# Optimization experiments

Hardware: AMD Instinct MI355X
Metric: run time of the kernel (lower is better)

Reference implementation:

```python
import jax, jax.numpy as jnp
import numpy as np

EMBED_DIM = 1024
NUM_HEADS = 16
HEAD_DIM = EMBED_DIM // NUM_HEADS


def setup_inputs() -> dict:
    key = jax.random.key(0)
    ks = jax.random.split(key, 9)
    B, S, D = 2, 2048, EMBED_DIM
    scale = 1.0 / np.sqrt(D)
    x = jax.random.normal(ks[0], (B, S, D), dtype=jnp.float32)
    # nn.Linear weights are [out, in]; store as [in, out] for x @ W
    Wq = jax.random.uniform(ks[1], (D, D), jnp.float32, -scale, scale)
    bq = jax.random.uniform(ks[2], (D,), jnp.float32, -scale, scale)
    Wk = jax.random.uniform(ks[3], (D, D), jnp.float32, -scale, scale)
    bk = jax.random.uniform(ks[4], (D,), jnp.float32, -scale, scale)
    Wv = jax.random.uniform(ks[5], (D, D), jnp.float32, -scale, scale)
    bv = jax.random.uniform(ks[6], (D,), jnp.float32, -scale, scale)
    Wo = jax.random.uniform(ks[7], (D, D), jnp.float32, -scale, scale)
    bo = jax.random.uniform(ks[8], (D,), jnp.float32, -scale, scale)
    return {"x": x, "Wq": Wq, "bq": bq, "Wk": Wk, "bk": bk,
            "Wv": Wv, "bv": bv, "Wo": Wo, "bo": bo}


def reference(x, Wq, bq, Wk, bk, Wv, bv, Wo, bo):
    B, S, D = x.shape
    H, Dh = NUM_HEADS, HEAD_DIM
    q = (x @ Wq + bq).reshape(B, S, H, Dh).transpose(0, 2, 1, 3)  # [B,H,S,Dh]
    k = (x @ Wk + bk).reshape(B, S, H, Dh).transpose(0, 2, 1, 3)
    v = (x @ Wv + bv).reshape(B, S, H, Dh).transpose(0, 2, 1, 3)
    scores = jnp.einsum('bhqd,bhkd->bhqk', q, k) / jnp.sqrt(jnp.float32(Dh))
    attn = jax.nn.softmax(scores, axis=-1)
    out = jnp.einsum('bhqk,bhkd->bhqd', attn, v)  # [B,H,S,Dh]
    out = out.transpose(0, 2, 1, 3).reshape(B, S, D)
    return out @ Wo + bo
```

## Files before the change

kernel.cpp:

```cpp
#include <hip/hip_runtime.h>
#include <hip/hip_bf16.h>
#include <stdint.h>

using f32x4 = __attribute__((ext_vector_type(4))) float;
using s16x8 = __attribute__((ext_vector_type(8))) short;
using s16x4 = __attribute__((ext_vector_type(4))) short;

__device__ __forceinline__ unsigned short f2bf(float f) {
  union { float f; unsigned int u; } v; v.f = f;
  return (unsigned short)((v.u + 0x7FFFu + ((v.u >> 16) & 1u)) >> 16);
}

__device__ __forceinline__ float exp2_(float x) {
  float r;
  asm("v_exp_f32 %0, %1" : "=v"(r) : "v"(x));
  return r;
}

__device__ __forceinline__ s16x4 pk4(float a, float b, float c, float d) {
  union { unsigned u[2]; s16x4 v; } r;
  asm("v_cvt_pk_bf16_f32 %0, %1, %2" : "=v"(r.u[0]) : "v"(a), "v"(b));
  asm("v_cvt_pk_bf16_f32 %0, %1, %2" : "=v"(r.u[1]) : "v"(c), "v"(d));
  return r.v;
}

__device__ __forceinline__ short pbf(float f) {
  __hip_bfloat16 h = __float2bfloat16(f);
  return *(short*)&h;
}

#define GLD16(gp, lp) __builtin_amdgcn_global_load_lds( \
    (const __attribute__((address_space(1))) unsigned int*)(uintptr_t)(gp), \
    (__attribute__((address_space(3))) unsigned int*)(uintptr_t)(lp), 16, 0, 0)

__device__ __forceinline__ f32x4 mfma32(s16x8 a, s16x8 b, f32x4 c) {
  return __builtin_amdgcn_mfma_f32_16x16x32_bf16(a, b, c, 0, 0, 0);
}

#if __has_builtin(__builtin_amdgcn_mfma_f32_16x16x16bf16_1k)
__device__ __forceinline__ f32x4 mfma16(s16x4 a, s16x4 b, f32x4 c) {
  return __builtin_amdgcn_mfma_f32_16x16x16bf16_1k(a, b, c, 0, 0, 0);
}
#else
__device__ __forceinline__ f32x4 mfma16(s16x4 a, s16x4 b, f32x4 c) {
  f32x4 d;
  asm volatile("v_mfma_f32_16x16x16_bf16 %0, %1, %2, %3"
               : "=v"(d) : "v"(a), "v"(b), "v"(c));
  return d;
}
#endif

__global__ __launch_bounds__(256)
void prep(const float* __restrict__ x,
          const float* __restrict__ Wq, const float* __restrict__ Wk,
          const float* __restrict__ Wv, const float* __restrict__ Wo,
          unsigned short* __restrict__ xb, unsigned short* __restrict__ Wt) {
  __shared__ float tile[64][65];
  int blk = blockIdx.x;
  int tid = threadIdx.x;
  if (blk < 1024) {
    const float4* xi = (const float4*)x;
    ushort4* xo = (ushort4*)xb;
    #pragma unroll
    for (int j = 0; j < 4; ++j) {
      int i = blk * 1024 + j * 256 + tid;
      float4 v = xi[i];
      ushort4 o;
      o.x = f2bf(v.x); o.y = f2bf(v.y); o.z = f2bf(v.z); o.w = f2bf(v.w);
      xo[i] = o;
    }
  } else {
    int wid = blk - 1024;
    int which = wid >> 8, t = wid & 255;
    const float* W = (which == 0) ? Wq : (which == 1) ? Wk : (which == 2) ? Wv : Wo;
    unsigned short* dst = Wt + (size_t)which * 1048576;
    int k0 = (t & 15) * 64, n0 = (t >> 4) * 64;
    int tx = tid & 63, ty = tid >> 6;
    #pragma unroll
    for (int j = 0; j < 64; j += 4)
      tile[ty + j][tx] = W[(size_t)(k0 + ty + j) * 1024 + n0 + tx];
    __syncthreads();
    #pragma unroll
    for (int j = 0; j < 64; j += 4)
      dst[(size_t)(n0 + ty + j) * 1024 + k0 + tx] = f2bf(tile[tx][ty + j]);
  }
}

__global__ __launch_bounds__(512, 2)
void qkv_gemm(const unsigned short* __restrict__ A,
              const unsigned short* __restrict__ Bt,
              const float* __restrict__ bq, const float* __restrict__ bk,
              const float* __restrict__ bv,
              unsigned short* __restrict__ qo, unsigned short* __restrict__ kf,
              unsigned short* __restrict__ vf) {
  __shared__ unsigned short lds2[2][28672];
  int orig = blockIdx.x;
  int wg = (orig & 7) * 32 + (orig >> 3);
  int bm = wg >> 4, bn = wg & 15;
  int m0 = bm << 8;
  int n0 = bn * 192;
  int tid = threadIdx.x;
  int w = tid >> 6, ln = tid & 63;
  int g = ln >> 4, c = ln & 15;
  int wm = w >> 2, wn = w & 3;

  int rrs = tid >> 3;
  int lcol = (((tid & 7) ^ ((tid >> 3) & 7)) << 4);
  const char* pA = (const char*)A + (size_t)(m0 + rrs) * 2048 + lcol;
  const char* pB = (const char*)Bt + (size_t)(n0 + rrs) * 2048 + lcol;
  int woff = w * 1024;

#define QKV_STAGE(buf, kt)                                                     \
  {                                                                            \
    char* db = (char*)&lds2[buf][0];                                           \
    _Pragma("unroll")                                                          \
    for (int s = 0; s < 4; ++s)                                                \
      GLD16(pA + (size_t)s * 131072 + (kt) * 128, db + s * 8192 + woff);       \
    _Pragma("unroll")                                                          \
    for (int s = 0; s < 3; ++s)                                                \
      GLD16(pB + (size_t)s * 131072 + (kt) * 128,                              \
            db + 32768 + s * 8192 + woff);                                     \
  }

  int cs = (c & 7) << 4;
#define DSFA(LA, mi, kk)                                                       \
  (*(const s16x8*)&(LA)[((mi) >> 2) * 4096 + (((mi) & 3) * 16 + c) * 64 +      \
                        ((((kk) * 64 + g * 16) ^ cs) >> 1)])
#define DSFB(LB, ni, kk)                                                       \
  (*(const s16x8*)&(LB)[((wn * 48 + (ni) * 16) >> 6) * 4096 +                  \
                        (((wn * 48 + (ni) * 16) & 63) + c) * 64 +              \
                        ((((kk) * 64 + g * 16) ^ cs) >> 1)])

  f32x4 acc[8][3];
  f32x4 zero = {0.f, 0.f, 0.f, 0.f};
  #pragma unroll
  for (int mi = 0; mi < 8; ++mi)
    #pragma unroll
    for (int ni = 0; ni < 3; ++ni) acc[mi][ni] = zero;

  QKV_STAGE(0, 0);
  asm volatile("s_waitcnt vmcnt(0)" ::: "memory");
  __builtin_amdgcn_s_barrier();

  for (int kt = 0; kt < 16; ++kt) {
    int bsel = kt & 1;
    const unsigned short* LA = &lds2[bsel][wm * 8192];
    const unsigned short* LB = &lds2[bsel][16384];
    if (kt < 15) QKV_STAGE(bsel ^ 1, kt + 1);

    s16x8 bfr[3][2];
    #pragma unroll
    for (int ni = 0; ni < 3; ++ni) {
      bfr[ni][0] = DSFB(LB, ni, 0);
      bfr[ni][1] = DSFB(LB, ni, 1);
    }
    s16x8 a[4][2];
    #pragma unroll
    for (int mi = 0; mi < 4; ++mi) {
      a[mi][0] = DSFA(LA, mi, 0);
      a[mi][1] = DSFA(LA, mi, 1);
    }
    __builtin_amdgcn_s_setprio(1);
    #pragma unroll
    for (int mi = 0; mi < 4; ++mi)
      #pragma unroll
      for (int ni = 0; ni < 3; ++ni) {
        acc[mi][ni] = mfma32(a[mi][0], bfr[ni][0], acc[mi][ni]);
        acc[mi][ni] = mfma32(a[mi][1], bfr[ni][1], acc[mi][ni]);
      }
    __builtin_amdgcn_s_setprio(0);
    #pragma unroll
    for (int mi = 0; mi < 4; ++mi) {
      a[mi][0] = DSFA(LA, mi + 4, 0);
      a[mi][1] = DSFA(LA, mi + 4, 1);
    }
    __builtin_amdgcn_s_setprio(1);
    #pragma unroll
    for (int mi = 0; mi < 4; ++mi)
      #pragma unroll
      for (int ni = 0; ni < 3; ++ni) {
        acc[mi + 4][ni] = mfma32(a[mi][0], bfr[ni][0], acc[mi + 4][ni]);
        acc[mi + 4][ni] = mfma32(a[mi][1], bfr[ni][1], acc[mi + 4][ni]);
      }
    __builtin_amdgcn_s_setprio(0);

    asm volatile("s_waitcnt vmcnt(0)" ::: "memory");
    __builtin_amdgcn_s_barrier();
  }
#undef QKV_STAGE
#undef DSFA
#undef DSFB

  #pragma unroll
  for (int ni = 0; ni < 3; ++ni) {
    int cg = n0 + wn * 48 + ni * 16 + c;
    int p = cg >> 10;
    int d = cg & 1023;
    int hh = d >> 6, dh = d & 63;
    const float* bp = (p == 0) ? bq : (p == 1) ? bk : bv;
    float bias = bp[d];
    #pragma unroll
    for (int mi = 0; mi < 8; ++mi) {
      int r = m0 + wm * 128 + mi * 16 + g * 4;
      int b2 = r >> 11, s = r & 2047;
      size_t pv = (size_t)((b2 << 4) + hh);
      if (p == 2) {
        int T = s >> 4;
        int Tp = T >> 1, par = T & 1;
        int dtp = dh >> 4;
        ushort4 pk;
        pk.x = f2bf(acc[mi][ni][0] + bias);
        pk.y = f2bf(acc[mi][ni][1] + bias);
        pk.z = f2bf(acc[mi][ni][2] + bias);
        pk.w = f2bf(acc[mi][ni][3] + bias);
        *(ushort4*)&vf[pv * 131072 +
                       (size_t)(((Tp * 4 + dtp) * 64 + g * 16 + c) * 8 + par * 4)] = pk;
      } else if (p == 1) {
        int T = s >> 4;
        int h2 = dh >> 5, gp = (dh >> 3) & 3, j = dh & 7;
        unsigned short* kd = kf + pv * 131072 + T * 1024 + h2 * 512 +
                             (gp * 16 + (s & 15)) * 8 + j;
        kd[0]  = f2bf(acc[mi][ni][0] + bias);
        kd[8]  = f2bf(acc[mi][ni][1] + bias);
        kd[16] = f2bf(acc[mi][ni][2] + bias);
        kd[24] = f2bf(acc[mi][ni][3] + bias);
      } else {
        const float sc = 0.180336880111120f;
        size_t base = (pv * 2048 + s) * 64 + dh;
        qo[base]       = f2bf((acc[mi][ni][0] + bias) * sc);
        qo[base + 64]  = f2bf((acc[mi][ni][1] + bias) * sc);
        qo[base + 128] = f2bf((acc[mi][ni][2] + bias) * sc);
        qo[base + 192] = f2bf((acc[mi][ni][3] + bias) * sc);
      }
    }
  }
}

__global__ __launch_bounds__(256, 2)
void attn_fwd(const unsigned short* __restrict__ q,
              const unsigned short* __restrict__ kfb,
              const unsigned short* __restrict__ vfb,
              unsigned short* __restrict__ ao) {
  __shared__ unsigned short ldsKV[3][8192];
  int orig = blockIdx.x;
  int wg = (orig & 7) * 64 + (orig >> 3);
  int pair = wg >> 4, qt = wg & 15;
  int tid = threadIdx.x;
  int w = tid >> 6, ln = tid & 63;
  int g = ln >> 4, c = ln & 15;
  int q0 = qt * 128 + w * 32;
  const unsigned short* qp = q + (size_t)pair * 131072;
  const char* kbase = (const char*)(kfb + (size_t)pair * 131072);
  const char* vbase = (const char*)(vfb + (size_t)pair * 131072);

  const char* ssrc = ((w < 2) ? kbase : vbase) + (w & 1) * 4096;
  int dsto = (w >= 2 ? 8192 : 0) + (w & 1) * 4096;

  s16x8 qf[2][2];
  #pragma unroll
  for (int j = 0; j < 2; ++j)
    #pragma unroll
    for (int h = 0; h < 2; ++h)
      qf[j][h] = *(const s16x8*)&qp[(q0 + j * 16 + c) * 64 + h * 32 + g * 8];

  f32x4 acc[2][4];
  f32x4 zero = {0.f, 0.f, 0.f, 0.f};
  #pragma unroll
  for (int j = 0; j < 2; ++j)
    #pragma unroll
    for (int dt = 0; dt < 4; ++dt) acc[j][dt] = zero;
  float l0 = 0.f, l1 = 0.f;

  #pragma unroll
  for (int j = 0; j < 4; ++j)
    GLD16(ssrc + j * 1024 + ln * 16, (char*)&ldsKV[0][0] + dsto + j * 1024);

  const unsigned short* L0 = ldsKV[0];
  const unsigned short* L1 = ldsKV[1];
  const unsigned short* L2 = ldsKV[2];
  s16x4 paA[2][4], paB[2][4];

#define ATTN_ITER(T, LC, LP, LN, PAC, PAP)                                     \
  {                                                                            \
    if ((T) < 31) {                                                            \
      const char* s2 = ssrc + ((T) + 1) * 8192;                                \
      char* d2 = (char*)(LN) + dsto;                                           \
      _Pragma("unroll")                                                        \
      for (int j = 0; j < 4; ++j)                                              \
        GLD16(s2 + j * 1024 + ln * 16, d2 + j * 1024);                         \
      asm volatile("s_waitcnt vmcnt(4)" ::: "memory");                         \
    } else {                                                                   \
      asm volatile("s_waitcnt vmcnt(0)" ::: "memory");                         \
    }                                                                          \
    __builtin_amdgcn_s_barrier();                                              \
    s16x8 kc[4][2];                                                            \
    _Pragma("unroll")                                                          \
    for (int kt = 0; kt < 4; ++kt) {                                           \
      kc[kt][0] = *(const s16x8*)&(LC)[kt * 1024 + ln * 8];                    \
      kc[kt][1] = *(const s16x8*)&(LC)[kt * 1024 + 512 + ln * 8];              \
    }                                                                          \
    f32x4 st[4][2];                                                            \
    __builtin_amdgcn_s_setprio(1);                                             \
    _Pragma("unroll")                                                          \
    for (int kt = 0; kt < 4; ++kt)                                             \
      _Pragma("unroll")                                                        \
      for (int j = 0; j < 2; ++j) {                                            \
        f32x4 t2 = zero;                                                       \
        t2 = mfma32(kc[kt][0], qf[j][0], t2);                                  \
        t2 = mfma32(kc[kt][1], qf[j][1], t2);                                  \
        st[kt][j] = t2;                                                        \
      }                                                                        \
    __builtin_amdgcn_s_setprio(0);                                             \
    if ((T) > 0) {                                                             \
      __builtin_amdgcn_s_setprio(1);                                           \
      _Pragma("unroll")                                                        \
      for (int dt = 0; dt < 4; ++dt)                                           \
        _Pragma("unroll")                                                      \
        for (int tp = 0; tp < 2; ++tp) {                                       \
          s16x8 vv = *(const s16x8*)&(LP)[4096 + tp * 2048 + dt * 512 + ln * 8]; \
          s16x4 vlo = __builtin_shufflevector(vv, vv, 0, 1, 2, 3);             \
          s16x4 vhi = __builtin_shufflevector(vv, vv, 4, 5, 6, 7);             \
          _Pragma("unroll")                                                    \
          for (int j = 0; j < 2; ++j) {                                        \
            acc[j][dt] = mfma16((PAP)[j][tp * 2], vlo, acc[j][dt]);            \
            acc[j][dt] = mfma16((PAP)[j][tp * 2 + 1], vhi, acc[j][dt]);        \
          }                                                                    \
        }                                                                      \
      __builtin_amdgcn_s_setprio(0);                                           \
    }                                                                          \
    _Pragma("unroll")                                                          \
    for (int kt = 0; kt < 4; ++kt) {                                           \
      float p00 = exp2_(st[kt][0][0]), p01 = exp2_(st[kt][0][1]);              \
      float p02 = exp2_(st[kt][0][2]), p03 = exp2_(st[kt][0][3]);              \
      float p10 = exp2_(st[kt][1][0]), p11 = exp2_(st[kt][1][1]);              \
      float p12 = exp2_(st[kt][1][2]), p13 = exp2_(st[kt][1][3]);              \
      l0 += (p00 + p01) + (p02 + p03);                                         \
      l1 += (p10 + p11) + (p12 + p13);                                         \
      (PAC)[0][kt] = pk4(p00, p01, p02, p03);                                  \
      (PAC)[1][kt] = pk4(p10, p11, p12, p13);                                  \
    }                                                                          \
    __builtin_amdgcn_s_barrier();                                              \
  }

  for (int t = 0; t < 32; t += 2) {
    ATTN_ITER(t,     L0, L2, L1, paA, paB);
    ATTN_ITER(t + 1, L1, L0, L2, paB, paA);
    const unsigned short* tmp = L2;
    L2 = L1; L1 = L0; L0 = tmp;
  }
#undef ATTN_ITER

  __builtin_amdgcn_s_setprio(1);
  #pragma unroll
  for (int dt = 0; dt < 4; ++dt)
    #pragma unroll
    for (int tp = 0; tp < 2; ++tp) {
      s16x8 vv = *(const s16x8*)&L2[4096 + tp * 2048 + dt * 512 + ln * 8];
      s16x4 vlo = __builtin_shufflevector(vv, vv, 0, 1, 2, 3);
      s16x4 vhi = __builtin_shufflevector(vv, vv, 4, 5, 6, 7);
      #pragma unroll
      for (int j = 0; j < 2; ++j) {
        acc[j][dt] = mfma16(paB[j][tp * 2], vlo, acc[j][dt]);
        acc[j][dt] = mfma16(paB[j][tp * 2 + 1], vhi, acc[j][dt]);
      }
    }
  __builtin_amdgcn_s_setprio(0);

  l0 += __shfl_xor(l0, 16); l0 += __shfl_xor(l0, 32);
  l1 += __shfl_xor(l1, 16); l1 += __shfl_xor(l1, 32);
  float li0 = 1.f / l0, li1 = 1.f / l1;
  int b = pair >> 4, hh = pair & 15;
  #pragma unroll
  for (int e = 0; e < 4; ++e) {
    float i0 = __shfl(li0, g * 4 + e);
    float i1 = __shfl(li1, g * 4 + e);
    size_t r0 = ((size_t)(b * 2048 + q0 + g * 4 + e) * 16 + hh) * 64;
    size_t r1 = ((size_t)(b * 2048 + q0 + 16 + g * 4 + e) * 16 + hh) * 64;
    #pragma unroll
    for (int dt = 0; dt < 4; ++dt) {
      ao[r0 + dt * 16 + c] = (unsigned short)pbf(acc[0][dt][e] * i0);
      ao[r1 + dt * 16 + c] = (unsigned short)pbf(acc[1][dt][e] * i1);
    }
  }
}

__global__ __launch_bounds__(256)
void out_gemm(const unsigned short* __restrict__ A,
              const unsigned short* __restrict__ Bt,
              const float* __restrict__ bo, float* __restrict__ out) {
  __shared__ unsigned short lds[2][6144];
  int orig = blockIdx.x;
  int wg = (orig & 7) * 64 + (orig >> 3);
  int bm = wg >> 3, bn = wg & 7;
  int m0 = bm << 6, n0 = bn << 7;
  int tid = threadIdx.x;
  int w = tid >> 6, ln = tid & 63;
  int g = ln >> 4, c = ln & 15;
  int wr = w >> 1, wc = w & 1;

  const unsigned short* su[3];
  int du[3];
  #pragma unroll
  for (int i = 0; i < 3; ++i) {
    int u = 3 * w + i;
    if (u < 4) {
      su[i] = A + (size_t)(m0 + u * 16 + (ln >> 2)) * 1024 + (ln & 3) * 8;
      du[i] = u * 512;
    } else {
      int v2 = u - 4;
      su[i] = Bt + (size_t)(n0 + v2 * 16 + (ln >> 2)) * 1024 + (ln & 3) * 8;
      du[i] = 2048 + v2 * 512;
    }
  }

  f32x4 acc[2][4];
  f32x4 zero = {0.f, 0.f, 0.f, 0.f};
  #pragma unroll
  for (int m = 0; m < 2; ++m)
    #pragma unroll
    for (int n = 0; n < 4; ++n) acc[m][n] = zero;

  #pragma unroll
  for (int i = 0; i < 3; ++i) GLD16(su[i], &lds[0][du[i]]);
  __syncthreads();

  int aoff = (wr * 32 + c) * 32 + g * 8;
  int boff = 2048 + (wc * 64 + c) * 32 + g * 8;

  int cur = 0;
  for (int t = 0; t < 32; ++t) {
    if (t < 31) {
      int nb = cur ^ 1;
      #pragma unroll
      for (int i = 0; i < 3; ++i) GLD16(su[i] + (t + 1) * 32, &lds[nb][du[i]]);
    }
    s16x8 af[2], bf[4];
    #pragma unroll
    for (int m = 0; m < 2; ++m)
      af[m] = *(const s16x8*)&lds[cur][aoff + m * 512];
    #pragma unroll
    for (int n = 0; n < 4; ++n)
      bf[n] = *(const s16x8*)&lds[cur][boff + n * 512];
    #pragma unroll
    for (int m = 0; m < 2; ++m)
      #pragma unroll
      for (int n = 0; n < 4; ++n)
        acc[m][n] = mfma32(af[m], bf[n], acc[m][n]);
    __syncthreads();
    cur ^= 1;
  }

  #pragma unroll
  for (int n = 0; n < 4; ++n) {
    int cg = n0 + wc * 64 + n * 16 + c;
    float bias = bo[cg];
    #pragma unroll
    for (int m = 0; m < 2; ++m) {
      int r = m0 + wr * 32 + m * 16 + g * 4;
      out[(size_t)r * 1024 + cg] = acc[m][n][0] + bias;
      out[(size_t)(r + 1) * 1024 + cg] = acc[m][n][1] + bias;
      out[(size_t)(r + 2) * 1024 + cg] = acc[m][n][2] + bias;
      out[(size_t)(r + 3) * 1024 + cg] = acc[m][n][3] + bias;
    }
  }
}

extern "C" void kernel_launch(void* const* d_in, const int* in_sizes, int n_in,
                              void* d_out, int out_size, void* d_ws, size_t ws_size,
                              hipStream_t stream) {
  (void)in_sizes; (void)n_in; (void)out_size; (void)ws_size;
  const float* x  = (const float*)d_in[0];
  const float* Wq = (const float*)d_in[1];
  const float* bq = (const float*)d_in[2];
  const float* Wk = (const float*)d_in[3];
  const float* bk = (const float*)d_in[4];
  const float* Wv = (const float*)d_in[5];
  const float* bv = (const float*)d_in[6];
  const float* Wo = (const float*)d_in[7];
  const float* bo = (const float*)d_in[8];
  float* out = (float*)d_out;
  char* ws = (char*)d_ws;
  unsigned short* xb  = (unsigned short*)(ws);
  unsigned short* Wt  = (unsigned short*)(ws + 8388608);
  unsigned short* Wot = (unsigned short*)(ws + 14680064);
  unsigned short* qb  = (unsigned short*)(ws + 16777216);
  unsigned short* kfb = (unsigned short*)(ws + 25165824);
  unsigned short* vfb = (unsigned short*)(ws + 33554432);
  unsigned short* ao  = (unsigned short*)(ws + 41943040);

  prep<<<2048, 256, 0, stream>>>(x, Wq, Wk, Wv, Wo, xb, Wt);
  qkv_gemm<<<256, 512, 0, stream>>>(xb, Wt, bq, bk, bv, qb, kfb, vfb);
  attn_fwd<<<512, 256, 0, stream>>>(qb, kfb, vfb, ao);
  out_gemm<<<512, 256, 0, stream>>>(ao, Wot, bo, out);
}
```

Before: 103.8 us.

## Use 16x16x32 bf16 MFMA for PV with cross-lane P shuffle

Replaces the pairs of 16x16x16 MFMAs in the P·V product with single 16x16x32 MFMAs. This halves the MFMA instruction count for that stage. The V fragment layout written by the QKV projection is changed to match the wider K dimension. The softmax probabilities are packed and redistributed across lanes with __shfl so each lane holds an 8-element A operand. That adds eight ds_bpermute-style shuffles and selects per fragment in the inner loop.

```diff
diff --git a/kernel.cpp b/kernel.cpp
--- a/kernel.cpp
+++ b/kernel.cpp
@@ -17,11 +17,10 @@
   return r;
 }
 
-__device__ __forceinline__ s16x4 pk4(float a, float b, float c, float d) {
-  union { unsigned u[2]; s16x4 v; } r;
-  asm("v_cvt_pk_bf16_f32 %0, %1, %2" : "=v"(r.u[0]) : "v"(a), "v"(b));
-  asm("v_cvt_pk_bf16_f32 %0, %1, %2" : "=v"(r.u[1]) : "v"(c), "v"(d));
-  return r.v;
+__device__ __forceinline__ unsigned cvtpk(float a, float b) {
+  unsigned r;
+  asm("v_cvt_pk_bf16_f32 %0, %1, %2" : "=v"(r) : "v"(a), "v"(b));
+  return r;
 }
 
 __device__ __forceinline__ short pbf(float f) {
@@ -36,19 +35,6 @@
 __device__ __forceinline__ f32x4 mfma32(s16x8 a, s16x8 b, f32x4 c) {
   return __builtin_amdgcn_mfma_f32_16x16x32_bf16(a, b, c, 0, 0, 0);
 }
-
-#if __has_builtin(__builtin_amdgcn_mfma_f32_16x16x16bf16_1k)
-__device__ __forceinline__ f32x4 mfma16(s16x4 a, s16x4 b, f32x4 c) {
-  return __builtin_amdgcn_mfma_f32_16x16x16bf16_1k(a, b, c, 0, 0, 0);
-}
-#else
-__device__ __forceinline__ f32x4 mfma16(s16x4 a, s16x4 b, f32x4 c) {
-  f32x4 d;
-  asm volatile("v_mfma_f32_16x16x16_bf16 %0, %1, %2, %3"
-               : "=v"(d) : "v"(a), "v"(b), "v"(c));
-  return d;
-}
-#endif
 
 __global__ __launch_bounds__(256)
 void prep(const float* __restrict__ x,
@@ -205,16 +191,16 @@
       int b2 = r >> 11, s = r & 2047;
       size_t pv = (size_t)((b2 << 4) + hh);
       if (p == 2) {
-        int T = s >> 4;
-        int Tp = T >> 1, par = T & 1;
-        int dtp = dh >> 4;
+        int ch = s >> 5;
+        int l16 = ((s >> 3) & 3) * 16 + (dh & 15);
+        int jo = s & 7;
         ushort4 pk;
         pk.x = f2bf(acc[mi][ni][0] + bias);
         pk.y = f2bf(acc[mi][ni][1] + bias);
         pk.z = f2bf(acc[mi][ni][2] + bias);
         pk.w = f2bf(acc[mi][ni][3] + bias);
         *(ushort4*)&vf[pv * 131072 +
-                       (size_t)(((Tp * 4 + dtp) * 64 + g * 16 + c) * 8 + par * 4)] = pk;
+                       (size_t)((ch * 4 + (dh >> 4)) * 64 + l16) * 8 + jo] = pk;
       } else if (p == 1) {
         int T = s >> 4;
         int h2 = dh >> 5, gp = (dh >> 3) & 3, j = dh & 7;
@@ -271,6 +257,10 @@
     for (int dt = 0; dt < 4; ++dt) acc[j][dt] = zero;
   float l0 = 0.f, l1 = 0.f;
 
+  int srcA = (g & 1) * 32 + c;
+  int srcB = srcA + 16;
+  int hi = g >> 1;
+
   #pragma unroll
   for (int j = 0; j < 4; ++j)
     GLD16(ssrc + j * 1024 + ln * 16, (char*)&ldsKV[0][0] + dsto + j * 1024);
@@ -278,7 +268,7 @@
   const unsigned short* L0 = ldsKV[0];
   const unsigned short* L1 = ldsKV[1];
   const unsigned short* L2 = ldsKV[2];
-  s16x4 paA[2][4], paB[2][4];
+  s16x8 paA[2][2], paB[2][2];
 
 #define ATTN_ITER(T, LC, LP, LN, PAC, PAP)                                     \
   {                                                                            \
@@ -314,20 +304,17 @@
     if ((T) > 0) {                                                             \
       __builtin_amdgcn_s_setprio(1);                                           \
       _Pragma("unroll")                                                        \
-      for (int dt = 0; dt < 4; ++dt)                                           \
+      for (int m = 0; m < 2; ++m)                                              \
         _Pragma("unroll")                                                      \
-        for (int tp = 0; tp < 2; ++tp) {                                       \
-          s16x8 vv = *(const s16x8*)&(LP)[4096 + tp * 2048 + dt * 512 + ln * 8]; \
-          s16x4 vlo = __builtin_shufflevector(vv, vv, 0, 1, 2, 3);             \
-          s16x4 vhi = __builtin_shufflevector(vv, vv, 4, 5, 6, 7);             \
+        for (int dt = 0; dt < 4; ++dt) {                                       \
+          s16x8 vv = *(const s16x8*)&(LP)[4096 + m * 2048 + dt * 512 + ln * 8];\
           _Pragma("unroll")                                                    \
-          for (int j = 0; j < 2; ++j) {                                        \
-            acc[j][dt] = mfma16((PAP)[j][tp * 2], vlo, acc[j][dt]);            \
-            acc[j][dt] = mfma16((PAP)[j][tp * 2 + 1], vhi, acc[j][dt]);        \
-          }                                                                    \
+          for (int j = 0; j < 2; ++j)                                          \
+            acc[j][dt] = mfma32((PAP)[j][m], vv, acc[j][dt]);                  \
         }                                                                      \
       __builtin_amdgcn_s_setprio(0);                                           \
     }                                                                          \
+    unsigned pu[2][4][2];                                                      \
     _Pragma("unroll")                                                          \
     for (int kt = 0; kt < 4; ++kt) {                                           \
       float p00 = exp2_(st[kt][0][0]), p01 = exp2_(st[kt][0][1]);              \
@@ -336,9 +323,28 @@
       float p12 = exp2_(st[kt][1][2]), p13 = exp2_(st[kt][1][3]);              \
       l0 += (p00 + p01) + (p02 + p03);                                         \
       l1 += (p10 + p11) + (p12 + p13);                                         \
-      (PAC)[0][kt] = pk4(p00, p01, p02, p03);                                  \
-      (PAC)[1][kt] = pk4(p10, p11, p12, p13);                                  \
+      pu[0][kt][0] = cvtpk(p00, p01); pu[0][kt][1] = cvtpk(p02, p03);          \
+      pu[1][kt][0] = cvtpk(p10, p11); pu[1][kt][1] = cvtpk(p12, p13);          \
     }                                                                          \
+    _Pragma("unroll")                                                          \
+    for (int j = 0; j < 2; ++j)                                                \
+      _Pragma("unroll")                                                        \
+      for (int m = 0; m < 2; ++m) {                                            \
+        unsigned a0 = pu[j][2 * m][0], a1 = pu[j][2 * m][1];                   \
+        unsigned b0 = pu[j][2 * m + 1][0], b1 = pu[j][2 * m + 1][1];           \
+        unsigned x0 = (unsigned)__shfl((int)a0, srcA);                         \
+        unsigned y0 = (unsigned)__shfl((int)b0, srcA);                         \
+        unsigned x1 = (unsigned)__shfl((int)a1, srcA);                         \
+        unsigned y1 = (unsigned)__shfl((int)b1, srcA);                         \
+        unsigned x2 = (unsigned)__shfl((int)a0, srcB);                         \
+        unsigned y2 = (unsigned)__shfl((int)b0, srcB);                         \
+        unsigned x3 = (unsigned)__shfl((int)a1, srcB);                         \
+        unsigned y3 = (unsigned)__shfl((int)b1, srcB);                         \
+        union { unsigned u[4]; s16x8 v; } wv;                                  \
+        wv.u[0] = hi ? y0 : x0; wv.u[1] = hi ? y1 : x1;                        \
+        wv.u[2] = hi ? y2 : x2; wv.u[3] = hi ? y3 : x3;                        \
+        (PAC)[j][m] = wv.v;                                                    \
+      }                                                                        \
     __builtin_amdgcn_s_barrier();                                              \
   }
 
@@ -352,17 +358,13 @@
 
   __builtin_amdgcn_s_setprio(1);
   #pragma unroll
-  for (int dt = 0; dt < 4; ++dt)
-    #pragma unroll
-    for (int tp = 0; tp < 2; ++tp) {
-      s16x8 vv = *(const s16x8*)&L2[4096 + tp * 2048 + dt * 512 + ln * 8];
-      s16x4 vlo = __builtin_shufflevector(vv, vv, 0, 1, 2, 3);
-      s16x4 vhi = __builtin_shufflevector(vv, vv, 4, 5, 6, 7);
+  for (int m = 0; m < 2; ++m)
+    #pragma unroll
+    for (int dt = 0; dt < 4; ++dt) {
+      s16x8 vv = *(const s16x8*)&L2[4096 + m * 2048 + dt * 512 + ln * 8];
       #pragma unroll
-      for (int j = 0; j < 2; ++j) {
-        acc[j][dt] = mfma16(paB[j][tp * 2], vlo, acc[j][dt]);
-        acc[j][dt] = mfma16(paB[j][tp * 2 + 1], vhi, acc[j][dt]);
-      }
+      for (int j = 0; j < 2; ++j)
+        acc[j][dt] = mfma32(paB[j][m], vv, acc[j][dt]);
     }
   __builtin_amdgcn_s_setprio(0);
 
```

Measured after the change: 115.3 us. +11.0%, slower.
